# Optimization experiments

Hardware: AMD Instinct MI355X
Metric: run time of the kernel (lower is better)

The kernel has to match this reference:

```python
import jax, jax.numpy as jnp
import numpy as np

TOL = 1e-3
LAM = 0.1          # Charbonnier lambda (lambda_ init kwarg)
MAX_ITER = 10


def cubic(x):
    ax = jnp.abs(x)
    ax2 = ax * ax
    ax3 = ax2 * ax
    return jnp.where(ax <= 1.0, 1.5 * ax3 - 2.5 * ax2 + 1.0,
                     jnp.where(ax < 2.0, -0.5 * ax3 + 2.5 * ax2 - 4.0 * ax + 2.0,
                               jnp.zeros_like(x)))


def bicubic_warp(I2, p):
    # Separable bicubic resampling on a translated grid (transform = TRANSLATION).
    B, H, W, C = I2.shape
    tx, ty = p[:, 0], p[:, 1]
    gx = jnp.arange(W, dtype=I2.dtype)[None, :] + tx[:, None]   # [B,W]
    gy = jnp.arange(H, dtype=I2.dtype)[None, :] + ty[:, None]   # [B,H]
    x0 = jnp.floor(gx).astype(jnp.int32)
    y0 = jnp.floor(gy).astype(jnp.int32)
    dx = gx - x0.astype(I2.dtype)
    dy = gy - y0.astype(I2.dtype)
    wx = jnp.stack([cubic(dx + 1.0), cubic(dx), cubic(dx - 1.0), cubic(dx - 2.0)], -1)  # [B,W,4]
    wy = jnp.stack([cubic(dy + 1.0), cubic(dy), cubic(dy - 1.0), cubic(dy - 2.0)], -1)  # [B,H,4]

    def tap(img, yj, xi):           # img [H,W,C], yj [H], xi [W]
        return img[yj][:, xi]       # [H,W,C] gather of one bicubic tap

    out = jnp.zeros_like(I2)
    for j in range(4):              # 16 fixed taps (i,j) of the 4x4 bicubic stencil
        yj = jnp.clip(y0 - 1 + j, 0, H - 1)
        for i in range(4):
            xi = jnp.clip(x0 - 1 + i, 0, W - 1)
            pix = jax.vmap(tap)(I2, yj, xi)                    # [B,H,W,C]
            w = wy[:, :, j][:, :, None] * wx[:, None, :, i]    # [B,H,W]
            out = out + pix * w[..., None]
    return out


def image_grads(I1):
    # central differences, zero-padded at borders (matches compute_gradients)
    Ix = jnp.pad((I1[:, :, 2:, :] - I1[:, :, :-2, :]) * 0.5,
                 ((0, 0), (0, 0), (1, 1), (0, 0)))
    Iy = jnp.pad((I1[:, 2:, :, :] - I1[:, :-2, :, :]) * 0.5,
                 ((0, 0), (1, 1), (0, 0), (0, 0)))
    return Ix, Iy


def setup_inputs() -> dict:
    key = jax.random.key(0)
    k1, k2, k3 = jax.random.split(key, 3)
    B, H, W, C = 16, 512, 512, 1
    I1 = jax.random.uniform(k1, (B, H, W, C), dtype=jnp.float32)
    I2 = jax.random.uniform(k2, (B, H, W, C), dtype=jnp.float32)
    p = jax.random.normal(k3, (B, 2), dtype=jnp.float32)
    return {"I1": I1, "I2": I2, "p": p}


def reference(I1, I2, p):
    Ix, Iy = image_grads(I1)
    # Translation Jacobian: Jx=[1,0], Jy=[0,1]  =>  steepest-descent images
    DIJ = jnp.stack([Ix, Iy], axis=-1)          # [B,H,W,C,2]

    def gn_step(carry, _):
        p_cur, err = carry
        Iw = bicubic_warp(I2, p_cur)
        DI = Iw - I1                            # [B,H,W,C]
        # Charbonnier robust weight per pixel
        rho = jax.lax.rsqrt(DI * DI + LAM * LAM)
        Hm = jnp.einsum('bhwcn,bhwc,bhwcm->bnm', DIJ, rho, DIJ)   # [B,2,2]
        bv = jnp.einsum('bhwcn,bhwc->bn', DIJ, DI * rho)          # [B,2]
        dp = jnp.einsum('bnm,bm->bn', jnp.linalg.inv(Hm), bv)
        active = err > TOL                      # emulate while_loop early-stop
        p_new = jnp.where(active, p_cur - dp, p_cur)
        err_new = jnp.where(active, jnp.linalg.norm(dp), err)
        return (p_new, err_new), None

    init = (p, jnp.asarray(1e10, jnp.float32))
    (p_final, final_error), _ = jax.lax.scan(gn_step, init, None, length=MAX_ITER)
    Iw_final = bicubic_warp(I2, p_final)
    DI_final = Iw_final - I1
    return p_final, final_error, DI_final, Iw_final
```

## Files before the change

### kernel.cpp

```cpp
#include <hip/hip_runtime.h>
#include <math.h>

#define NB 16
#define NH 512
#define NW 512
#define NHW (NH * NW)
#define LAM2 0.01f
#define TOLV 0.001f
#define MAXIT 10
#define ROWS 16
#define RPW 4
#define NCHUNK (NH / ROWS)
#define NTHREADS 256
#define COMP_STRIDE (NB * NCHUNK)

#define PARTIALS_N (5 * NB * NCHUNK)
#define PWS_OFF (PARTIALS_N * 8)
#define ERR_OFF (PWS_OFF + 32 * 4)

__device__ __forceinline__ float cubicf(float t) {
    float a = fabsf(t);
    float a2 = a * a;
    float a3 = a2 * a;
    if (a <= 1.0f) return 1.5f * a3 - 2.5f * a2 + 1.0f;
    if (a < 2.0f)  return -0.5f * a3 + 2.5f * a2 - 4.0f * a + 2.0f;
    return 0.0f;
}

__device__ __forceinline__ int clampy(int v) { return min(max(v, 0), NH - 1); }
__device__ __forceinline__ int clampx(int v) { return min(max(v, 0), NW - 1); }

__device__ __forceinline__ float4 L4(const float* __restrict__ p, int row, int i) {
    return ((const float4*)(p + (size_t)row * NW))[i];
}

__device__ __forceinline__ void unpack8(const float4& A, const float4& B, float* o) {
    o[0] = A.x; o[1] = A.y; o[2] = A.z; o[3] = A.w;
    o[4] = B.x; o[5] = B.y; o[6] = B.z; o[7] = B.w;
}

__device__ __forceinline__ void decode_bid(int bid, int& b, int& strip) {
    b = (bid & 7) + ((bid >> 8) << 3);
    strip = (bid >> 3) & 31;
}

__global__ __launch_bounds__(64) void gn_init(const float* __restrict__ p_in,
                                              float* __restrict__ pws,
                                              float* __restrict__ errws) {
    int t = threadIdx.x;
    if (t < 2 * NB) pws[t] = p_in[t];
    if (t == 0) errws[0] = 1e10f;
}

__global__ __launch_bounds__(NTHREADS) void gn_reduce(const float* __restrict__ I1,
                                                      const float* __restrict__ I2,
                                                      const float* __restrict__ pws,
                                                      double* __restrict__ partials) {
    int b, strip;
    decode_bid(blockIdx.x, b, strip);
    const int tid = threadIdx.x;
    const int wv = tid >> 6, lane = tid & 63;
    const int c0 = 8 * lane;
    const float tx = pws[2 * b];
    const float ty = pws[2 * b + 1];
    const float* I1b = I1 + (size_t)b * NHW;
    const float* I2b = I2 + (size_t)b * NHW;

    float gx0 = (float)c0 + tx;
    float fx0 = floorf(gx0);
    float dx0 = gx0 - fx0;
    int x00 = (int)fx0;
    const float wx0 = cubicf(dx0 + 1.0f), wx1 = cubicf(dx0);
    const float wx2 = cubicf(dx0 - 1.0f), wx3 = cubicf(dx0 - 2.0f);
    bool fast = true;
#pragma unroll
    for (int j = 1; j < 8; ++j) {
        int xj = (int)floorf((float)(c0 + j) + tx);
        fast = fast && (xj == x00 + j);
    }
    const int base = x00 - 1;
    fast = fast && (base >= -8) && (base + 10 <= NW + 7);
    const int s = base & 3;
    const int wbase = base - s;

    __shared__ float VS[4][NW + 24];
    float* Vw = VS[wv];

    const int ybase = strip * ROWS + wv * RPW;

    int yj0, yj1, yj2, yj3;
    {
        int yy = (int)floorf((float)ybase + ty);
        yj0 = clampy(yy - 1); yj1 = clampy(yy);
        yj2 = clampy(yy + 1); yj3 = clampy(yy + 2);
    }
    float4 w0a = L4(I2b, yj0, 2 * lane), w0b = L4(I2b, yj0, 2 * lane + 1);
    float4 w1a = L4(I2b, yj1, 2 * lane), w1b = L4(I2b, yj1, 2 * lane + 1);
    float4 w2a = L4(I2b, yj2, 2 * lane), w2b = L4(I2b, yj2, 2 * lane + 1);
    float4 w3a = L4(I2b, yj3, 2 * lane), w3b = L4(I2b, yj3, 2 * lane + 1);

    float4 cpa = L4(I1b, max(ybase - 1, 0), 2 * lane), cpb = L4(I1b, max(ybase - 1, 0), 2 * lane + 1);
    float4 cca = L4(I1b, ybase, 2 * lane),             ccb = L4(I1b, ybase, 2 * lane + 1);
    float4 cna = L4(I1b, min(ybase + 1, NH - 1), 2 * lane), cnb = L4(I1b, min(ybase + 1, NH - 1), 2 * lane + 1);

    float a0 = 0.f, a1 = 0.f, a2 = 0.f, a3 = 0.f, a4 = 0.f;

#pragma unroll
    for (int r = 0; r < RPW; ++r) {
        const int y = ybase + r;

        float gy = (float)y + ty, fy = floorf(gy), dy = gy - fy;
        const float wy0 = cubicf(dy + 1.0f), wy1 = cubicf(dy);
        const float wy2 = cubicf(dy - 1.0f), wy3 = cubicf(dy - 2.0f);

        int nyj0 = 0, nyj1 = 0, nyj2 = 0, nyj3 = 0;
        bool aligned = true;
        float4 nta, ntb, n1a, n1b;
        if (r + 1 < RPW) {
            int yy2 = (int)floorf((float)(y + 1) + ty);
            nyj0 = clampy(yy2 - 1); nyj1 = clampy(yy2);
            nyj2 = clampy(yy2 + 1); nyj3 = clampy(yy2 + 2);
            aligned = (nyj0 == yj1) && (nyj1 == yj2) && (nyj2 == yj3);
            nta = L4(I2b, nyj3, 2 * lane); ntb = L4(I2b, nyj3, 2 * lane + 1);
            n1a = L4(I1b, min(y + 2, NH - 1), 2 * lane);
            n1b = L4(I1b, min(y + 2, NH - 1), 2 * lane + 1);
        }

        float4 Va, Vb;
        Va.x = wy0 * w0a.x + wy1 * w1a.x + wy2 * w2a.x + wy3 * w3a.x;
        Va.y = wy0 * w0a.y + wy1 * w1a.y + wy2 * w2a.y + wy3 * w3a.y;
        Va.z = wy0 * w0a.z + wy1 * w1a.z + wy2 * w2a.z + wy3 * w3a.z;
        Va.w = wy0 * w0a.w + wy1 * w1a.w + wy2 * w2a.w + wy3 * w3a.w;
        Vb.x = wy0 * w0b.x + wy1 * w1b.x + wy2 * w2b.x + wy3 * w3b.x;
        Vb.y = wy0 * w0b.y + wy1 * w1b.y + wy2 * w2b.y + wy3 * w3b.y;
        Vb.z = wy0 * w0b.z + wy1 * w1b.z + wy2 * w2b.z + wy3 * w3b.z;
        Vb.w = wy0 * w0b.w + wy1 * w1b.w + wy2 * w2b.w + wy3 * w3b.w;
        ((float4*)(Vw + 8))[2 * lane] = Va;
        ((float4*)(Vw + 8))[2 * lane + 1] = Vb;
        if (lane == 0)  { float4 h; h.x = h.y = h.z = h.w = Va.x; ((float4*)Vw)[0] = h; ((float4*)Vw)[1] = h; }
        if (lane == 63) { float4 h; h.x = h.y = h.z = h.w = Vb.w; ((float4*)(Vw + 8 + NW))[0] = h; ((float4*)(Vw + 8 + NW))[1] = h; }

        float left = __shfl_up(ccb.w, 1);
        float right = __shfl_down(cca.x, 1);
        float cc[8], cp[8], cn[8];
        unpack8(cca, ccb, cc); unpack8(cpa, cpb, cp); unpack8(cna, cnb, cn);
        float Ix[8], Iy[8];
        Ix[0] = (lane > 0) ? 0.5f * (cc[1] - left) : 0.0f;
#pragma unroll
        for (int j = 1; j < 7; ++j) Ix[j] = 0.5f * (cc[j + 1] - cc[j - 1]);
        Ix[7] = (lane < 63) ? 0.5f * (right - cc[6]) : 0.0f;
        const bool yint = (y >= 1 && y <= NH - 2);
#pragma unroll
        for (int j = 0; j < 8; ++j) Iy[j] = yint ? 0.5f * (cn[j] - cp[j]) : 0.0f;

        float Hc[8];
        if (fast) {
            const float4* Wp = (const float4*)(Vw + 8 + wbase);
            float4 W0 = Wp[0], W1 = Wp[1], W2 = Wp[2], W3 = Wp[3];
            float u0, u1, u2, u3, u4, u5, u6, u7, u8, u9, u10;
            switch (s) {
                case 0:  u0=W0.x; u1=W0.y; u2=W0.z; u3=W0.w; u4=W1.x; u5=W1.y; u6=W1.z; u7=W1.w; u8=W2.x; u9=W2.y; u10=W2.z; break;
                case 1:  u0=W0.y; u1=W0.z; u2=W0.w; u3=W1.x; u4=W1.y; u5=W1.z; u6=W1.w; u7=W2.x; u8=W2.y; u9=W2.z; u10=W2.w; break;
                case 2:  u0=W0.z; u1=W0.w; u2=W1.x; u3=W1.y; u4=W1.z; u5=W1.w; u6=W2.x; u7=W2.y; u8=W2.z; u9=W2.w; u10=W3.x; break;
                default: u0=W0.w; u1=W1.x; u2=W1.y; u3=W1.z; u4=W1.w; u5=W2.x; u6=W2.y; u7=W2.z; u8=W2.w; u9=W3.x; u10=W3.y; break;
            }
            Hc[0] = wx0*u0 + wx1*u1 + wx2*u2  + wx3*u3;
            Hc[1] = wx0*u1 + wx1*u2 + wx2*u3  + wx3*u4;
            Hc[2] = wx0*u2 + wx1*u3 + wx2*u4  + wx3*u5;
            Hc[3] = wx0*u3 + wx1*u4 + wx2*u5  + wx3*u6;
            Hc[4] = wx0*u4 + wx1*u5 + wx2*u6  + wx3*u7;
            Hc[5] = wx0*u5 + wx1*u6 + wx2*u7  + wx3*u8;
            Hc[6] = wx0*u6 + wx1*u7 + wx2*u8  + wx3*u9;
            Hc[7] = wx0*u7 + wx1*u8 + wx2*u9  + wx3*u10;
        } else {
#pragma unroll
            for (int j = 0; j < 8; ++j) {
                float g = (float)(c0 + j) + tx;
                float f = floorf(g);
                int x0 = (int)f;
                float d = g - f;
                float v0 = cubicf(d + 1.0f), v1 = cubicf(d);
                float v2 = cubicf(d - 1.0f), v3 = cubicf(d - 2.0f);
                Hc[j] = v0 * Vw[8 + clampx(x0 - 1)] + v1 * Vw[8 + clampx(x0)] +
                        v2 * Vw[8 + clampx(x0 + 1)] + v3 * Vw[8 + clampx(x0 + 2)];
            }
        }

#pragma unroll
        for (int j = 0; j < 8; ++j) {
            float DI = Hc[j] - cc[j];
            float rho = 1.0f / sqrtf(DI * DI + LAM2);
            float dr = DI * rho;
            a0 += Ix[j] * Ix[j] * rho;
            a1 += Ix[j] * Iy[j] * rho;
            a2 += Iy[j] * Iy[j] * rho;
            a3 += Ix[j] * dr;
            a4 += Iy[j] * dr;
        }

        if (r + 1 < RPW) {
            if (aligned) {
                w0a = w1a; w0b = w1b; w1a = w2a; w1b = w2b; w2a = w3a; w2b = w3b;
            } else {
                w0a = L4(I2b, nyj0, 2 * lane); w0b = L4(I2b, nyj0, 2 * lane + 1);
                w1a = L4(I2b, nyj1, 2 * lane); w1b = L4(I2b, nyj1, 2 * lane + 1);
                w2a = L4(I2b, nyj2, 2 * lane); w2b = L4(I2b, nyj2, 2 * lane + 1);
            }
            w3a = nta; w3b = ntb;
            yj0 = nyj0; yj1 = nyj1; yj2 = nyj2; yj3 = nyj3;
            cpa = cca; cpb = ccb; cca = cna; ccb = cnb; cna = n1a; cnb = n1b;
        }
    }

    double d0 = a0, d1 = a1, d2 = a2, d3 = a3, d4 = a4;
#pragma unroll
    for (int off = 32; off > 0; off >>= 1) {
        d0 += __shfl_down(d0, off);
        d1 += __shfl_down(d1, off);
        d2 += __shfl_down(d2, off);
        d3 += __shfl_down(d3, off);
        d4 += __shfl_down(d4, off);
    }
    __shared__ double wsum[4][5];
    if (lane == 0) {
        wsum[wv][0] = d0; wsum[wv][1] = d1; wsum[wv][2] = d2;
        wsum[wv][3] = d3; wsum[wv][4] = d4;
    }
    __syncthreads();
    if (tid < 5) {
        double ssum = wsum[0][tid] + wsum[1][tid] + wsum[2][tid] + wsum[3][tid];
        partials[(size_t)tid * COMP_STRIDE + b * NCHUNK + strip] = ssum;
    }
}

__global__ __launch_bounds__(128) void gn_update(const double* __restrict__ partials,
                                                 float* __restrict__ pws,
                                                 float* __restrict__ errws,
                                                 float* __restrict__ out,
                                                 int write_out) {
    __shared__ double Hs[NB][5];
    __shared__ float dpf[NB][2];
    __shared__ float pnew[2 * NB];
    const int tid = threadIdx.x;

    if (tid < NB * 5) {
        int bb = tid & 15, comp = tid >> 4;
        const double* src = partials + (size_t)comp * COMP_STRIDE + bb * NCHUNK;
        double s = 0;
#pragma unroll 8
        for (int ch = 0; ch < NCHUNK; ++ch) s += src[ch];
        Hs[bb][comp] = s;
    }
    __syncthreads();

    if (tid < NB) {
        double H00 = Hs[tid][0], H01 = Hs[tid][1], H11 = Hs[tid][2];
        double b0 = Hs[tid][3], b1 = Hs[tid][4];
        double inv = 1.0 / (H00 * H11 - H01 * H01);
        double dp0 = ( H11 * b0 - H01 * b1) * inv;
        double dp1 = (-H01 * b0 + H00 * b1) * inv;
        dpf[tid][0] = (float)dp0;
        dpf[tid][1] = (float)dp1;
    }
    __syncthreads();

    float err_old = errws[0];
    bool active = err_old > TOLV;

    if (tid < 2 * NB) {
        float pv = pws[tid];
        if (active) pv -= dpf[tid >> 1][tid & 1];
        pnew[tid] = pv;
        pws[tid] = pv;
    }

    float err_new = err_old;
    if (tid == 0) {
        if (active) {
            double n = 0;
            for (int i = 0; i < NB; ++i) {
                n += (double)dpf[i][0] * (double)dpf[i][0];
                n += (double)dpf[i][1] * (double)dpf[i][1];
            }
            err_new = (float)sqrt(n);
            errws[0] = err_new;
        }
    }
    __syncthreads();
    if (write_out) {
        if (tid < 2 * NB) out[tid] = pnew[tid];
        if (tid == 0) out[2 * NB] = err_new;
    }
}

__global__ __launch_bounds__(NTHREADS) void gn_final(const float* __restrict__ I1,
                                                     const float* __restrict__ I2,
                                                     const float* __restrict__ pws,
                                                     float* __restrict__ out) {
    int b, strip;
    decode_bid(blockIdx.x, b, strip);
    const int tid = threadIdx.x;
    const int wv = tid >> 6, lane = tid & 63;
    const int c0 = 8 * lane;
    const float tx = pws[2 * b];
    const float ty = pws[2 * b + 1];
    const float* I1b = I1 + (size_t)b * NHW;
    const float* I2b = I2 + (size_t)b * NHW;

    float* DIout = out + 33;
    float* IWout = out + 33 + (size_t)NB * NHW;

    float gx0 = (float)c0 + tx;
    float fx0 = floorf(gx0);
    float dx0 = gx0 - fx0;
    int x00 = (int)fx0;
    const float wx0 = cubicf(dx0 + 1.0f), wx1 = cubicf(dx0);
    const float wx2 = cubicf(dx0 - 1.0f), wx3 = cubicf(dx0 - 2.0f);
    bool fast = true;
#pragma unroll
    for (int j = 1; j < 8; ++j) {
        int xj = (int)floorf((float)(c0 + j) + tx);
        fast = fast && (xj == x00 + j);
    }
    const int base = x00 - 1;
    fast = fast && (base >= -8) && (base + 10 <= NW + 7);
    const int s = base & 3;
    const int wbase = base - s;

    __shared__ float VS[4][NW + 24];
    float* Vw = VS[wv];

    const int ybase = strip * ROWS + wv * RPW;

    int yj0, yj1, yj2, yj3;
    {
        int yy = (int)floorf((float)ybase + ty);
        yj0 = clampy(yy - 1); yj1 = clampy(yy);
        yj2 = clampy(yy + 1); yj3 = clampy(yy + 2);
    }
    float4 w0a = L4(I2b, yj0, 2 * lane), w0b = L4(I2b, yj0, 2 * lane + 1);
    float4 w1a = L4(I2b, yj1, 2 * lane), w1b = L4(I2b, yj1, 2 * lane + 1);
    float4 w2a = L4(I2b, yj2, 2 * lane), w2b = L4(I2b, yj2, 2 * lane + 1);
    float4 w3a = L4(I2b, yj3, 2 * lane), w3b = L4(I2b, yj3, 2 * lane + 1);
    float4 cca = L4(I1b, ybase, 2 * lane), ccb = L4(I1b, ybase, 2 * lane + 1);

#pragma unroll
    for (int r = 0; r < RPW; ++r) {
        const int y = ybase + r;

        float gy = (float)y + ty, fy = floorf(gy), dy = gy - fy;
        const float wy0 = cubicf(dy + 1.0f), wy1 = cubicf(dy);
        const float wy2 = cubicf(dy - 1.0f), wy3 = cubicf(dy - 2.0f);

        int nyj0 = 0, nyj1 = 0, nyj2 = 0, nyj3 = 0;
        bool aligned = true;
        float4 nta, ntb, n1a, n1b;
        if (r + 1 < RPW) {
            int yy2 = (int)floorf((float)(y + 1) + ty);
            nyj0 = clampy(yy2 - 1); nyj1 = clampy(yy2);
            nyj2 = clampy(yy2 + 1); nyj3 = clampy(yy2 + 2);
            aligned = (nyj0 == yj1) && (nyj1 == yj2) && (nyj2 == yj3);
            nta = L4(I2b, nyj3, 2 * lane); ntb = L4(I2b, nyj3, 2 * lane + 1);
            n1a = L4(I1b, y + 1, 2 * lane); n1b = L4(I1b, y + 1, 2 * lane + 1);
        }

        float4 Va, Vb;
        Va.x = wy0 * w0a.x + wy1 * w1a.x + wy2 * w2a.x + wy3 * w3a.x;
        Va.y = wy0 * w0a.y + wy1 * w1a.y + wy2 * w2a.y + wy3 * w3a.y;
        Va.z = wy0 * w0a.z + wy1 * w1a.z + wy2 * w2a.z + wy3 * w3a.z;
        Va.w = wy0 * w0a.w + wy1 * w1a.w + wy2 * w2a.w + wy3 * w3a.w;
        Vb.x = wy0 * w0b.x + wy1 * w1b.x + wy2 * w2b.x + wy3 * w3b.x;
        Vb.y = wy0 * w0b.y + wy1 * w1b.y + wy2 * w2b.y + wy3 * w3b.y;
        Vb.z = wy0 * w0b.z + wy1 * w1b.z + wy2 * w2b.z + wy3 * w3b.z;
        Vb.w = wy0 * w0b.w + wy1 * w1b.w + wy2 * w2b.w + wy3 * w3b.w;
        ((float4*)(Vw + 8))[2 * lane] = Va;
        ((float4*)(Vw + 8))[2 * lane + 1] = Vb;
        if (lane == 0)  { float4 h; h.x = h.y = h.z = h.w = Va.x; ((float4*)Vw)[0] = h; ((float4*)Vw)[1] = h; }
        if (lane == 63) { float4 h; h.x = h.y = h.z = h.w = Vb.w; ((float4*)(Vw + 8 + NW))[0] = h; ((float4*)(Vw + 8 + NW))[1] = h; }

        float Hc[8];
        if (fast) {
            const float4* Wp = (const float4*)(Vw + 8 + wbase);
            float4 W0 = Wp[0], W1 = Wp[1], W2 = Wp[2], W3 = Wp[3];
            float u0, u1, u2, u3, u4, u5, u6, u7, u8, u9, u10;
            switch (s) {
                case 0:  u0=W0.x; u1=W0.y; u2=W0.z; u3=W0.w; u4=W1.x; u5=W1.y; u6=W1.z; u7=W1.w; u8=W2.x; u9=W2.y; u10=W2.z; break;
                case 1:  u0=W0.y; u1=W0.z; u2=W0.w; u3=W1.x; u4=W1.y; u5=W1.z; u6=W1.w; u7=W2.x; u8=W2.y; u9=W2.z; u10=W2.w; break;
                case 2:  u0=W0.z; u1=W0.w; u2=W1.x; u3=W1.y; u4=W1.z; u5=W1.w; u6=W2.x; u7=W2.y; u8=W2.z; u9=W2.w; u10=W3.x; break;
                default: u0=W0.w; u1=W1.x; u2=W1.y; u3=W1.z; u4=W1.w; u5=W2.x; u6=W2.y; u7=W2.z; u8=W2.w; u9=W3.x; u10=W3.y; break;
            }
            Hc[0] = wx0*u0 + wx1*u1 + wx2*u2  + wx3*u3;
            Hc[1] = wx0*u1 + wx1*u2 + wx2*u3  + wx3*u4;
            Hc[2] = wx0*u2 + wx1*u3 + wx2*u4  + wx3*u5;
            Hc[3] = wx0*u3 + wx1*u4 + wx2*u5  + wx3*u6;
            Hc[4] = wx0*u4 + wx1*u5 + wx2*u6  + wx3*u7;
            Hc[5] = wx0*u5 + wx1*u6 + wx2*u7  + wx3*u8;
            Hc[6] = wx0*u6 + wx1*u7 + wx2*u8  + wx3*u9;
            Hc[7] = wx0*u7 + wx1*u8 + wx2*u9  + wx3*u10;
        } else {
#pragma unroll
            for (int j = 0; j < 8; ++j) {
                float g = (float)(c0 + j) + tx;
                float f = floorf(g);
                int x0 = (int)f;
                float d = g - f;
                float v0 = cubicf(d + 1.0f), v1 = cubicf(d);
                float v2 = cubicf(d - 1.0f), v3 = cubicf(d - 2.0f);
                Hc[j] = v0 * Vw[8 + clampx(x0 - 1)] + v1 * Vw[8 + clampx(x0)] +
                        v2 * Vw[8 + clampx(x0 + 1)] + v3 * Vw[8 + clampx(x0 + 2)];
            }
        }

        float cc[8];
        unpack8(cca, ccb, cc);
        float4 dA, dB, wA, wB;
        dA.x = Hc[0] - cc[0]; dA.y = Hc[1] - cc[1]; dA.z = Hc[2] - cc[2]; dA.w = Hc[3] - cc[3];
        dB.x = Hc[4] - cc[4]; dB.y = Hc[5] - cc[5]; dB.z = Hc[6] - cc[6]; dB.w = Hc[7] - cc[7];
        wA.x = Hc[0]; wA.y = Hc[1]; wA.z = Hc[2]; wA.w = Hc[3];
        wB.x = Hc[4]; wB.y = Hc[5]; wB.z = Hc[6]; wB.w = Hc[7];
        size_t o = (size_t)b * NHW + (size_t)y * NW + c0;
        *(float4*)(DIout + o) = dA; *(float4*)(DIout + o + 4) = dB;
        *(float4*)(IWout + o) = wA; *(float4*)(IWout + o + 4) = wB;

        if (r + 1 < RPW) {
            if (aligned) {
                w0a = w1a; w0b = w1b; w1a = w2a; w1b = w2b; w2a = w3a; w2b = w3b;
            } else {
                w0a = L4(I2b, nyj0, 2 * lane); w0b = L4(I2b, nyj0, 2 * lane + 1);
                w1a = L4(I2b, nyj1, 2 * lane); w1b = L4(I2b, nyj1, 2 * lane + 1);
                w2a = L4(I2b, nyj2, 2 * lane); w2b = L4(I2b, nyj2, 2 * lane + 1);
            }
            w3a = nta; w3b = ntb;
            yj0 = nyj0; yj1 = nyj1; yj2 = nyj2; yj3 = nyj3;
            cca = n1a; ccb = n1b;
        }
    }
}

extern "C" void kernel_launch(void* const* d_in, const int* in_sizes, int n_in,
                              void* d_out, int out_size, void* d_ws, size_t ws_size,
                              hipStream_t stream) {
    const float* I1 = (const float*)d_in[0];
    const float* I2 = (const float*)d_in[1];
    const float* p  = (const float*)d_in[2];
    float* out = (float*)d_out;

    double* partials = (double*)d_ws;
    float* pws   = (float*)((char*)d_ws + PWS_OFF);
    float* errws = (float*)((char*)d_ws + ERR_OFF);

    gn_init<<<1, 64, 0, stream>>>(p, pws, errws);

    const int nblk = NCHUNK * NB;
    for (int t = 0; t < MAXIT; ++t) {
        gn_reduce<<<nblk, NTHREADS, 0, stream>>>(I1, I2, pws, partials);
        gn_update<<<1, 128, 0, stream>>>(partials, pws, errws, out, (t == MAXIT - 1) ? 1 : 0);
    }
    gn_final<<<nblk, NTHREADS, 0, stream>>>(I1, I2, pws, out);
}
```

Measured before the change: 181.4 us.

## Fuse Gauss-Newton parameter update into each reduction block, removing serial update launches

The single-block update kernel and the init kernel are removed. Every block of the next reduction (and of the final warp) now redundantly re-sums the previous step's partials, solves the 2x2 systems and applies the update itself. Partials and state are double-buffered by iteration parity so no block overwrites data another block is still reading. This cuts the launch count roughly in half and drops the tiny serial kernels, at the cost of each of 512 blocks reading 80x32 doubles and adding two block barriers before its main work.

```diff
diff --git a/kernel.cpp b/kernel.cpp
--- a/kernel.cpp
+++ b/kernel.cpp
@@ -13,10 +13,10 @@
 #define NCHUNK (NH / ROWS)
 #define NTHREADS 256
 #define COMP_STRIDE (NB * NCHUNK)
-
-#define PARTIALS_N (5 * NB * NCHUNK)
-#define PWS_OFF (PARTIALS_N * 8)
-#define ERR_OFF (PWS_OFF + 32 * 4)
+#define NBLK (NB * NCHUNK)
+
+#define PARTIALS_SLOT (5 * COMP_STRIDE)
+#define STATE_OFF_BYTES (2 * PARTIALS_SLOT * 8)
 
 __device__ __forceinline__ float cubicf(float t) {
     float a = fabsf(t);
@@ -44,27 +44,82 @@
     strip = (bid >> 3) & 31;
 }
 
-__global__ __launch_bounds__(64) void gn_init(const float* __restrict__ p_in,
-                                              float* __restrict__ pws,
-                                              float* __restrict__ errws) {
-    int t = threadIdx.x;
-    if (t < 2 * NB) pws[t] = p_in[t];
-    if (t == 0) errws[0] = 1e10f;
-}
-
-__global__ __launch_bounds__(NTHREADS) void gn_reduce(const float* __restrict__ I1,
-                                                      const float* __restrict__ I2,
-                                                      const float* __restrict__ pws,
-                                                      double* __restrict__ partials) {
+__device__ __forceinline__ void do_update(int t, int b, int tid,
+                                          const float* __restrict__ p_in,
+                                          const double* __restrict__ partials,
+                                          float* __restrict__ state,
+                                          float& px, float& py, float& err_out) {
+    if (t == 0) {
+        px = p_in[2 * b]; py = p_in[2 * b + 1];
+        err_out = 1e10f;
+        if (tid < 32) state[tid] = p_in[tid];
+        if (tid == 32) state[32] = 1e10f;
+        return;
+    }
+    __shared__ double HsS[NB][5];
+    __shared__ float dpfS[NB][2];
+    __shared__ float pst[33];
+    const double* src = partials + (size_t)((t - 1) & 1) * PARTIALS_SLOT;
+    const float* stp = state + ((t - 1) & 1) * 34;
+    float* stw = state + (t & 1) * 34;
+
+    if (tid < 33) pst[tid] = stp[tid];
+    if (tid < 80) {
+        const double* q = src + 32 * tid;
+        double s = 0;
+#pragma unroll
+        for (int ch = 0; ch < 32; ++ch) s += q[ch];
+        HsS[tid & 15][tid >> 4] = s;
+    }
+    __syncthreads();
+    if (tid < NB) {
+        double H00 = HsS[tid][0], H01 = HsS[tid][1], H11 = HsS[tid][2];
+        double b0 = HsS[tid][3], b1 = HsS[tid][4];
+        double inv = 1.0 / (H00 * H11 - H01 * H01);
+        dpfS[tid][0] = (float)(( H11 * b0 - H01 * b1) * inv);
+        dpfS[tid][1] = (float)((-H01 * b0 + H00 * b1) * inv);
+    }
+    __syncthreads();
+    float err_prev = pst[32];
+    bool active = err_prev > TOLV;
+    px = pst[2 * b]; py = pst[2 * b + 1];
+    if (active) { px -= dpfS[b][0]; py -= dpfS[b][1]; }
+    float err_new = err_prev;
+    if (active) {
+        double n = 0;
+        for (int i = 0; i < NB; ++i) {
+            n += (double)dpfS[i][0] * (double)dpfS[i][0];
+            n += (double)dpfS[i][1] * (double)dpfS[i][1];
+        }
+        err_new = (float)sqrt(n);
+    }
+    err_out = err_new;
+    if (tid < 32) {
+        float v = pst[tid];
+        if (active) v -= dpfS[tid >> 1][tid & 1];
+        stw[tid] = v;
+    }
+    if (tid == 32) stw[32] = err_new;
+    __syncthreads();
+}
+
+__global__ __launch_bounds__(NTHREADS) void gn_step(const float* __restrict__ I1,
+                                                    const float* __restrict__ I2,
+                                                    const float* __restrict__ p_in,
+                                                    double* __restrict__ partials,
+                                                    float* __restrict__ state,
+                                                    int t) {
     int b, strip;
     decode_bid(blockIdx.x, b, strip);
     const int tid = threadIdx.x;
     const int wv = tid >> 6, lane = tid & 63;
     const int c0 = 8 * lane;
-    const float tx = pws[2 * b];
-    const float ty = pws[2 * b + 1];
     const float* I1b = I1 + (size_t)b * NHW;
     const float* I2b = I2 + (size_t)b * NHW;
+
+    float px, py, errv;
+    do_update(t, b, tid, p_in, partials, state, px, py, errv);
+    const float tx = px, ty = py;
 
     float gx0 = (float)c0 + tx;
     float fx0 = floorf(gx0);
@@ -85,7 +140,6 @@
 
     __shared__ float VS[4][NW + 24];
     float* Vw = VS[wv];
-
     const int ybase = strip * ROWS + wv * RPW;
 
     int yj0, yj1, yj2, yj3;
@@ -227,85 +281,33 @@
         wsum[wv][3] = d3; wsum[wv][4] = d4;
     }
     __syncthreads();
+    double* pb = partials + (size_t)(t & 1) * PARTIALS_SLOT;
     if (tid < 5) {
         double ssum = wsum[0][tid] + wsum[1][tid] + wsum[2][tid] + wsum[3][tid];
-        partials[(size_t)tid * COMP_STRIDE + b * NCHUNK + strip] = ssum;
-    }
-}
-
-__global__ __launch_bounds__(128) void gn_update(const double* __restrict__ partials,
-                                                 float* __restrict__ pws,
-                                                 float* __restrict__ errws,
-                                                 float* __restrict__ out,
-                                                 int write_out) {
-    __shared__ double Hs[NB][5];
-    __shared__ float dpf[NB][2];
-    __shared__ float pnew[2 * NB];
-    const int tid = threadIdx.x;
-
-    if (tid < NB * 5) {
-        int bb = tid & 15, comp = tid >> 4;
-        const double* src = partials + (size_t)comp * COMP_STRIDE + bb * NCHUNK;
-        double s = 0;
-#pragma unroll 8
-        for (int ch = 0; ch < NCHUNK; ++ch) s += src[ch];
-        Hs[bb][comp] = s;
-    }
-    __syncthreads();
-
-    if (tid < NB) {
-        double H00 = Hs[tid][0], H01 = Hs[tid][1], H11 = Hs[tid][2];
-        double b0 = Hs[tid][3], b1 = Hs[tid][4];
-        double inv = 1.0 / (H00 * H11 - H01 * H01);
-        double dp0 = ( H11 * b0 - H01 * b1) * inv;
-        double dp1 = (-H01 * b0 + H00 * b1) * inv;
-        dpf[tid][0] = (float)dp0;
-        dpf[tid][1] = (float)dp1;
-    }
-    __syncthreads();
-
-    float err_old = errws[0];
-    bool active = err_old > TOLV;
-
-    if (tid < 2 * NB) {
-        float pv = pws[tid];
-        if (active) pv -= dpf[tid >> 1][tid & 1];
-        pnew[tid] = pv;
-        pws[tid] = pv;
-    }
-
-    float err_new = err_old;
-    if (tid == 0) {
-        if (active) {
-            double n = 0;
-            for (int i = 0; i < NB; ++i) {
-                n += (double)dpf[i][0] * (double)dpf[i][0];
-                n += (double)dpf[i][1] * (double)dpf[i][1];
-            }
-            err_new = (float)sqrt(n);
-            errws[0] = err_new;
-        }
-    }
-    __syncthreads();
-    if (write_out) {
-        if (tid < 2 * NB) out[tid] = pnew[tid];
-        if (tid == 0) out[2 * NB] = err_new;
+        pb[(size_t)tid * COMP_STRIDE + b * NCHUNK + strip] = ssum;
     }
 }
 
 __global__ __launch_bounds__(NTHREADS) void gn_final(const float* __restrict__ I1,
                                                      const float* __restrict__ I2,
-                                                     const float* __restrict__ pws,
+                                                     const float* __restrict__ p_in,
+                                                     double* __restrict__ partials,
+                                                     float* __restrict__ state,
                                                      float* __restrict__ out) {
     int b, strip;
     decode_bid(blockIdx.x, b, strip);
     const int tid = threadIdx.x;
     const int wv = tid >> 6, lane = tid & 63;
     const int c0 = 8 * lane;
-    const float tx = pws[2 * b];
-    const float ty = pws[2 * b + 1];
     const float* I1b = I1 + (size_t)b * NHW;
     const float* I2b = I2 + (size_t)b * NHW;
+
+    float px, py, errv;
+    do_update(MAXIT, b, tid, p_in, partials, state, px, py, errv);
+    const float tx = px, ty = py;
+
+    if (strip == 0 && tid == 0) { out[2 * b] = px; out[2 * b + 1] = py; }
+    if (blockIdx.x == 0 && tid == 0) out[2 * NB] = errv;
 
     float* DIout = out + 33;
     float* IWout = out + 33 + (size_t)NB * NHW;
@@ -329,7 +331,6 @@
 
     __shared__ float VS[4][NW + 24];
     float* Vw = VS[wv];
-
     const int ybase = strip * ROWS + wv * RPW;
 
     int yj0, yj1, yj2, yj3;
@@ -444,17 +445,11 @@
     const float* I2 = (const float*)d_in[1];
     const float* p  = (const float*)d_in[2];
     float* out = (float*)d_out;
-
     double* partials = (double*)d_ws;
-    float* pws   = (float*)((char*)d_ws + PWS_OFF);
-    float* errws = (float*)((char*)d_ws + ERR_OFF);
-
-    gn_init<<<1, 64, 0, stream>>>(p, pws, errws);
-
-    const int nblk = NCHUNK * NB;
+    float* state = (float*)((char*)d_ws + STATE_OFF_BYTES);
+
     for (int t = 0; t < MAXIT; ++t) {
-        gn_reduce<<<nblk, NTHREADS, 0, stream>>>(I1, I2, pws, partials);
-        gn_update<<<1, 128, 0, stream>>>(partials, pws, errws, out, (t == MAXIT - 1) ? 1 : 0);
-    }
-    gn_final<<<nblk, NTHREADS, 0, stream>>>(I1, I2, pws, out);
-}
+        gn_step<<<NBLK, NTHREADS, 0, stream>>>(I1, I2, p, partials, state, t);
+    }
+    gn_final<<<NBLK, NTHREADS, 0, stream>>>(I1, I2, p, partials, state, out);
+}
```

After: 160.3 us. -11.6%, faster.
